# Optimization experiments

Hardware: AMD Instinct MI355X
Metric: run time of the kernel (lower is better)

## Reference

```python
import jax, jax.numpy as jnp
import numpy as np

B, T, H, I, O = 2048, 256, 256, 64, 64  # batch, seq_len, hidden, input(=output) dim


def setup_inputs() -> dict:
    key = jax.random.key(0)
    ks = jax.random.split(key, 14)
    def w(k, shape, fan):
        return jax.random.normal(k, shape, jnp.float32) / np.float32(np.sqrt(fan))
    return {
        "noise": jax.random.normal(ks[0], (B, I), jnp.float32),
        "W_ih0": w(ks[1], (3 * H, I), I),
        "W_hh0": w(ks[2], (3 * H, H), H),
        "b_ih0": w(ks[3], (3 * H,), H),
        "b_hh0": w(ks[4], (3 * H,), H),
        "W_ih12": w(ks[5], (2, 3 * H, H), H),
        "W_hh12": w(ks[6], (2, 3 * H, H), H),
        "b_ih12": w(ks[7], (2, 3 * H), H),
        "b_hh12": w(ks[8], (2, 3 * H), H),
        "W1": w(ks[9], (H, H), H),
        "b1": w(ks[10], (H,), H),
        "W2": w(ks[11], (O, H), H),
        "b2": w(ks[12], (O,), H),
        "seq_len": T,
    }


def _gru_cell(x, h, Wi, Wh, bi, bh):
    # PyTorch GRU cell, gate order (r, z, n)
    gi = x @ Wi.T + bi        # [B, 3H]
    gh = h @ Wh.T + bh        # [B, 3H]
    ir, iz, inn = jnp.split(gi, 3, axis=-1)
    hr, hz, hn = jnp.split(gh, 3, axis=-1)
    r = jax.nn.sigmoid(ir + hr)
    z = jax.nn.sigmoid(iz + hz)
    n = jnp.tanh(inn + r * hn)
    return (1.0 - z) * n + z * h


def reference(noise, W_ih0, W_hh0, b_ih0, b_hh0, W_ih12, W_hh12, b_ih12, b_hh12,
              W1, b1, W2, b2, seq_len):
    Bb = noise.shape[0]
    Hd = W_hh0.shape[1]
    h_init = jnp.zeros((3, Bb, Hd), noise.dtype)

    def step(carry, _):
        x, h = carry
        h0 = _gru_cell(x, h[0], W_ih0, W_hh0, b_ih0, b_hh0)
        h1 = _gru_cell(h0, h[1], W_ih12[0], W_hh12[0], b_ih12[0], b_hh12[0])
        h2 = _gru_cell(h1, h[2], W_ih12[1], W_hh12[1], b_ih12[1], b_hh12[1])
        # output MLP: Linear -> ReLU -> Linear -> Tanh; fed back as next input
        y = jnp.tanh(jax.nn.relu(h2 @ W1.T + b1) @ W2.T + b2)  # [B, O]
        return (y, jnp.stack([h0, h1, h2])), y

    _, ys = jax.lax.scan(step, (noise, h_init), None, length=seq_len)
    return jnp.transpose(ys, (1, 0, 2))  # [B, T, O]
```

## Files before the change

kernel.cpp:

```cpp
#include <hip/hip_runtime.h>
#include <hip/hip_bf16.h>


typedef __attribute__((ext_vector_type(8))) short short8;
typedef __attribute__((ext_vector_type(4))) float f32x4;

#define TT   256
#define NTHR 512
#define NBLK 256

#define FB_WI0  0
#define FB_WH0  6144
#define FB_WI1  30720
#define FB_WH1  55296
#define FB_WI2  79872
#define FB_WH2  104448
#define FB_W1   129024
#define FB_W2   137216
#define TOTAL_FRAGS 139264

#define OFF_FLAGS 2228224u
#define OFF_H0    (OFF_FLAGS + 4096u)
#define OFF_H1    (OFF_H0 + 1048576u)
#define OFF_H2    (OFF_H1 + 1048576u)
#define OFF_A1    (OFF_H2 + 1048576u)
#define OFF_Y     (OFF_A1 + 1048576u)

#define WH0_F 0
#define WI1_F 24
#define WH1_F 48
#define WI2_F 72
#define WH2_F 96
#define W2_F  120
#define XW_F  152

__device__ __forceinline__ short bf16_rne(float v) {
  union { float f; unsigned u; } c; c.f = v;
  unsigned u = c.u;
  u += 0x7FFFu + ((u >> 16) & 1u);
  return (short)(u >> 16);
}
__device__ __forceinline__ float fast_sigmoid(float x) {
  return 1.0f / (1.0f + __expf(-x));
}
__device__ __forceinline__ float fast_tanh(float x) {
  return 1.0f - 2.0f / (__expf(2.0f * x) + 1.0f);
}

__device__ __forceinline__ void gll(const short* src, short* ldst) {
  __builtin_amdgcn_global_load_lds(
      (const __attribute__((address_space(1))) void*)src,
      (__attribute__((address_space(3))) void*)ldst, 16, 0, 0);
}
__device__ __forceinline__ void vm0() {
  asm volatile("s_waitcnt vmcnt(0)" ::: "memory");
  __builtin_amdgcn_sched_barrier(0);
}

__device__ __forceinline__ void gstore_ic(short* g, short v) {
  asm volatile("global_store_short %0, %1, off sc0 sc1" :: "v"(g), "v"(v) : "memory");
}

__device__ __forceinline__ void gather8_ic(const short* base, short8 (&f)[8]) {
  asm volatile(
      "global_load_dwordx4 %0, %8, off sc0 sc1\n\t"
      "global_load_dwordx4 %1, %8, off offset:64 sc0 sc1\n\t"
      "global_load_dwordx4 %2, %8, off offset:128 sc0 sc1\n\t"
      "global_load_dwordx4 %3, %8, off offset:192 sc0 sc1\n\t"
      "global_load_dwordx4 %4, %8, off offset:256 sc0 sc1\n\t"
      "global_load_dwordx4 %5, %8, off offset:320 sc0 sc1\n\t"
      "global_load_dwordx4 %6, %8, off offset:384 sc0 sc1\n\t"
      "global_load_dwordx4 %7, %8, off offset:448 sc0 sc1\n\t"
      "s_waitcnt vmcnt(0)"
      : "=&v"(f[0]), "=&v"(f[1]), "=&v"(f[2]), "=&v"(f[3]),
        "=&v"(f[4]), "=&v"(f[5]), "=&v"(f[6]), "=&v"(f[7])
      : "v"(base) : "memory");
}

__device__ __forceinline__ void gather2_l2(const short* base, short8& a, short8& b) {
  asm volatile(
      "global_load_dwordx4 %0, %2, off sc0\n\t"
      "global_load_dwordx4 %1, %2, off offset:64 sc0\n\t"
      "s_waitcnt vmcnt(0)"
      : "=&v"(a), "=&v"(b) : "v"(base) : "memory");
}

__device__ __forceinline__ void flag_add(unsigned* f) {
  unsigned one = 1u;
  asm volatile("global_atomic_add %0, %1, off sc1" :: "v"(f), "v"(one) : "memory");
}
__device__ __forceinline__ unsigned flag_read(unsigned* f) {
  unsigned v;
  asm volatile("global_load_dword %0, %1, off sc0 sc1\n\ts_waitcnt vmcnt(0)"
               : "=&v"(v) : "v"(f) : "memory");
  return v;
}

__device__ __forceinline__ void group_sync(unsigned* flag, unsigned target) {
  vm0();
  __syncthreads();
  if (threadIdx.x == 0) {
    flag_add(flag);
    while (flag_read(flag) < target) __builtin_amdgcn_s_sleep(1);
  }
  __syncthreads();
}

struct CB4 { float brz, bzz, bin, bhn; };
__device__ __forceinline__ CB4 make_cb4(const float* bi, const float* bh, int col) {
  CB4 cb;
  cb.brz = bi[col] + bh[col];
  cb.bzz = bi[256 + col] + bh[256 + col];
  cb.bin = bi[512 + col];
  cb.bhn = bh[512 + col];
  return cb;
}

__global__ void pack_weights(const float* __restrict__ Wi0, const float* __restrict__ Wh0,
                             const float* __restrict__ Wih12, const float* __restrict__ Whh12,
                             const float* __restrict__ W1, const float* __restrict__ W2,
                             short* __restrict__ outp)
{
  int f = blockIdx.x * blockDim.x + threadIdx.x;
  if (f >= TOTAL_FRAGS) return;
  const float* src; int K; int rel;
  if (f < FB_WH0)        { src = Wi0;            K = 64;  rel = f; }
  else if (f < FB_WI1)   { src = Wh0;            K = 256; rel = f - FB_WH0; }
  else if (f < FB_WH1)   { src = Wih12;          K = 256; rel = f - FB_WI1; }
  else if (f < FB_WI2)   { src = Whh12;          K = 256; rel = f - FB_WH1; }
  else if (f < FB_WH2)   { src = Wih12 + 196608; K = 256; rel = f - FB_WI2; }
  else if (f < FB_W1)    { src = Whh12 + 196608; K = 256; rel = f - FB_WH2; }
  else if (f < FB_W2)    { src = W1;             K = 256; rel = f - FB_W1; }
  else                   { src = W2;             K = 256; rel = f - FB_W2; }
  int lane = rel & 63;
  int q = rel >> 6;
  int KT = K >> 5;
  int kt = q % KT;
  int nt = q / KT;
  int n  = nt * 16 + (lane & 15);
  int k0 = kt * 32 + (lane >> 4) * 8;
  short8 v;
#pragma unroll
  for (int e = 0; e < 8; ++e) v[e] = bf16_rne(src[(size_t)n * K + k0 + e]);
  *(short8*)(outp + (size_t)f * 8) = v;
}

__global__ void zero_flags(unsigned* f) {
  if (threadIdx.x < 1024) f[threadIdx.x] = 0u;
}

#define MFMA(a, b, acc) __builtin_amdgcn_mfma_f32_16x16x32_bf16((a), (b), (acc), 0, 0, 0)
#define LDSF(idx) (*(const short8*)(wlds + (idx) * 512 + lane * 8))

#define GATE_UPDATE(agi, agh, cb, hm, hg)                                    \
  _Pragma("unroll") for (int j = 0; j < 4; ++j) {                            \
    float r_ = fast_sigmoid(agi[0][j] + agh[0][j] + cb.brz);                 \
    float z_ = fast_sigmoid(agi[1][j] + agh[1][j] + cb.bzz);                 \
    float n_ = fast_tanh(agi[2][j] + cb.bin + r_ * (agh[2][j] + cb.bhn));    \
    float h_ = n_ + z_ * (hm[j] - n_);                                       \
    hm[j] = h_;                                                              \
    gstore_ic(hg + (size_t)(grow0 + lhi * 4 + j) * 256 + col, bf16_rne(h_)); \
  }

__global__ __launch_bounds__(NTHR, 2)
void timegan_shard(const float* __restrict__ noise, char* __restrict__ ws,
                   const float* __restrict__ b_ih0, const float* __restrict__ b_hh0,
                   const float* __restrict__ b_ih12, const float* __restrict__ b_hh12,
                   const float* __restrict__ b1v, const float* __restrict__ b2v,
                   float* __restrict__ out)
{
  __shared__ __align__(16) short wlds[158 * 512];

  const short* wpack = (const short*)ws;
  unsigned* flags = (unsigned*)(ws + OFF_FLAGS);
  short* h0g = (short*)(ws + OFF_H0);
  short* h1g = (short*)(ws + OFF_H1);
  short* h2g = (short*)(ws + OFF_H2);
  short* a1g = (short*)(ws + OFF_A1);
  short* yg  = (short*)(ws + OFF_Y);

  const int tid = threadIdx.x;
  const int lane = tid & 63, w = tid >> 6;
  const int l15 = lane & 15, lhi = lane >> 4;
  const int gg = blockIdx.x & 15;
  const int m  = blockIdx.x >> 4;
  const int grow0 = gg * 128 + w * 16;
  const int col = m * 16 + l15;
  unsigned* gflag = flags + gg * 8;
  short* ybb = yg + (size_t)blockIdx.x * 128 * 64;

  if (w == 0) {
    int dst = 0;
    const int fbs[5] = {FB_WH0, FB_WI1, FB_WH1, FB_WI2, FB_WH2};
    for (int s = 0; s < 5; ++s)
      for (int g = 0; g < 3; ++g)
        for (int kt = 0; kt < 8; ++kt) {
          gll(wpack + ((size_t)fbs[s] + (size_t)((g * 16 + m) * 8 + kt) * 64 + lane) * 8,
              wlds + dst * 512);
          ++dst;
        }
    for (int nt = 0; nt < 4; ++nt)
      for (int kt = 0; kt < 8; ++kt) {
        gll(wpack + ((size_t)FB_W2 + (nt * 8 + kt) * 64 + lane) * 8, wlds + dst * 512);
        ++dst;
      }
    for (int g = 0; g < 3; ++g)
      for (int kt = 0; kt < 2; ++kt) {
        gll(wpack + ((size_t)FB_WI0 + ((g * 16 + m) * 2 + kt) * 64 + lane) * 8,
            wlds + dst * 512);
        ++dst;
      }
  }

  short8 w1f[8];
#pragma unroll
  for (int kt = 0; kt < 8; ++kt)
    w1f[kt] = *(const short8*)(wpack + ((size_t)FB_W1 + (m * 8 + kt) * 64 + lane) * 8);

  short8 xf[2];
  {
    const float* np = noise + (size_t)(grow0 + l15) * 64;
#pragma unroll
    for (int kt = 0; kt < 2; ++kt) {
      f32x4 u0 = *(const f32x4*)(np + kt * 32 + lhi * 8);
      f32x4 u1 = *(const f32x4*)(np + kt * 32 + lhi * 8 + 4);
      short8 v;
#pragma unroll
      for (int e = 0; e < 4; ++e) { v[e] = bf16_rne(u0[e]); v[4 + e] = bf16_rne(u1[e]); }
      xf[kt] = v;
    }
  }

  CB4 cb0 = make_cb4(b_ih0, b_hh0, col);
  CB4 cb1 = make_cb4(b_ih12, b_hh12, col);
  CB4 cb2 = make_cb4(b_ih12 + 768, b_hh12 + 768, col);
  float bm1 = b1v[col];
  float bm2v[4];
#pragma unroll
  for (int nt = 0; nt < 4; ++nt) bm2v[nt] = b2v[nt * 16 + l15];

  short8 h0f[8], h1f[8], h2f[8];
  float hm0[4], hm1[4], hm2[4];
  {
    short8 z8 = {0, 0, 0, 0, 0, 0, 0, 0};
#pragma unroll
    for (int kt = 0; kt < 8; ++kt) { h0f[kt] = z8; h1f[kt] = z8; h2f[kt] = z8; }
#pragma unroll
    for (int j = 0; j < 4; ++j) { hm0[j] = 0.f; hm1[j] = 0.f; hm2[j] = 0.f; }
  }

  vm0();
  __syncthreads();

  const f32x4 z4 = {0.f, 0.f, 0.f, 0.f};
  const int rowoff = (grow0 + l15) * 256 + lhi * 8;

#pragma unroll 1
  for (int t = 0; t < TT; ++t) {
    const unsigned tgt = 16u * (unsigned)(t + 1);

    {
      f32x4 agi[3] = {z4, z4, z4}, agh[3] = {z4, z4, z4};
#pragma unroll
      for (int g = 0; g < 3; ++g) {
        agi[g] = MFMA(xf[0], LDSF(XW_F + g * 2 + 0), agi[g]);
        agi[g] = MFMA(xf[1], LDSF(XW_F + g * 2 + 1), agi[g]);
      }
#pragma unroll
      for (int kt = 0; kt < 8; ++kt)
#pragma unroll
        for (int g = 0; g < 3; ++g)
          agh[g] = MFMA(h0f[kt], LDSF(WH0_F + g * 8 + kt), agh[g]);
      GATE_UPDATE(agi, agh, cb0, hm0, h0g)
    }
    group_sync(gflag + 0, tgt);
    gather8_ic(h0g + rowoff, h0f);

    {
      f32x4 agi[3] = {z4, z4, z4}, agh[3] = {z4, z4, z4};
#pragma unroll
      for (int kt = 0; kt < 8; ++kt)
#pragma unroll
        for (int g = 0; g < 3; ++g) {
          agi[g] = MFMA(h0f[kt], LDSF(WI1_F + g * 8 + kt), agi[g]);
          agh[g] = MFMA(h1f[kt], LDSF(WH1_F + g * 8 + kt), agh[g]);
        }
      GATE_UPDATE(agi, agh, cb1, hm1, h1g)
    }
    group_sync(gflag + 1, tgt);
    gather8_ic(h1g + rowoff, h1f);

    {
      f32x4 agi[3] = {z4, z4, z4}, agh[3] = {z4, z4, z4};
#pragma unroll
      for (int kt = 0; kt < 8; ++kt)
#pragma unroll
        for (int g = 0; g < 3; ++g) {
          agi[g] = MFMA(h1f[kt], LDSF(WI2_F + g * 8 + kt), agi[g]);
          agh[g] = MFMA(h2f[kt], LDSF(WH2_F + g * 8 + kt), agh[g]);
        }
      GATE_UPDATE(agi, agh, cb2, hm2, h2g)
    }
    group_sync(gflag + 2, tgt);
    gather8_ic(h2g + rowoff, h2f);

    {
      f32x4 am = z4;
#pragma unroll
      for (int kt = 0; kt < 8; ++kt) am = MFMA(h2f[kt], w1f[kt], am);
#pragma unroll
      for (int j = 0; j < 4; ++j) {
        float v = fmaxf(am[j] + bm1, 0.f);
        gstore_ic(a1g + (size_t)(grow0 + lhi * 4 + j) * 256 + col, bf16_rne(v));
      }
    }
    group_sync(gflag + 3, tgt);
    short8 af[8];
    gather8_ic(a1g + rowoff, af);

#pragma unroll
    for (int nt = 0; nt < 4; ++nt) {
      f32x4 ay = z4;
#pragma unroll
      for (int kt = 0; kt < 8; ++kt) ay = MFMA(af[kt], LDSF(W2_F + nt * 8 + kt), ay);
#pragma unroll
      for (int j = 0; j < 4; ++j) {
        int grow = grow0 + lhi * 4 + j;
        float y = fast_tanh(ay[j] + bm2v[nt]);
        if (m == 0) out[((size_t)grow * TT + t) * 64 + nt * 16 + l15] = y;
        ybb[(w * 16 + lhi * 4 + j) * 64 + nt * 16 + l15] = bf16_rne(y);
      }
    }
    if (t < TT - 1) {
      vm0();
      gather2_l2(ybb + (w * 16 + l15) * 64 + lhi * 8, xf[0], xf[1]);
    }
  }
}

extern "C" void kernel_launch(void* const* d_in, const int* in_sizes, int n_in,
                              void* d_out, int out_size, void* d_ws, size_t ws_size,
                              hipStream_t stream)
{
  const float* noise  = (const float*)d_in[0];
  const float* W_ih0  = (const float*)d_in[1];
  const float* W_hh0  = (const float*)d_in[2];
  const float* b_ih0  = (const float*)d_in[3];
  const float* b_hh0  = (const float*)d_in[4];
  const float* W_ih12 = (const float*)d_in[5];
  const float* W_hh12 = (const float*)d_in[6];
  const float* b_ih12 = (const float*)d_in[7];
  const float* b_hh12 = (const float*)d_in[8];
  const float* W1     = (const float*)d_in[9];
  const float* b1     = (const float*)d_in[10];
  const float* W2     = (const float*)d_in[11];
  const float* b2     = (const float*)d_in[12];
  float* out = (float*)d_out;
  char* ws = (char*)d_ws;
  short* wpack = (short*)d_ws;

  zero_flags<<<1, 1024, 0, stream>>>((unsigned*)(ws + OFF_FLAGS));
  pack_weights<<<(TOTAL_FRAGS + 255) / 256, 256, 0, stream>>>(
      W_ih0, W_hh0, W_ih12, W_hh12, W1, W2, wpack);

  timegan_shard<<<NBLK, NTHR, 0, stream>>>(
      noise, ws, b_ih0, b_hh0, b_ih12, b_hh12, b1, b2, out);
}
```

Measured before the change: 5.470 ms.

## Use XCC-local L2 atomics for group barriers when the group shares one XCC

At startup each block records its hardware XCC id. Each 16-block group then checks whether all its members run on the same XCC. If they do, the per-step barriers use device-scope L2 atomics (add plus an atomic read-back of zero) measured against a captured base value, instead of system-coherent atomics and bypassing loads. Flag counters are also spread to separate cache lines. This aims to cut the latency of the four inter-block barriers per timestep, at the cost of an extra init handshake and two template instantiations of the main loop.

After: 5.208 ms. 4.8% less time.

```diff
diff --git a/kernel.cpp b/kernel.cpp
--- a/kernel.cpp
+++ b/kernel.cpp
@@ -20,7 +20,7 @@
 #define TOTAL_FRAGS 139264
 
 #define OFF_FLAGS 2228224u
-#define OFF_H0    (OFF_FLAGS + 4096u)
+#define OFF_H0    (OFF_FLAGS + 16384u)
 #define OFF_H1    (OFF_H0 + 1048576u)
 #define OFF_H2    (OFF_H1 + 1048576u)
 #define OFF_A1    (OFF_H2 + 1048576u)
@@ -60,7 +60,6 @@
 __device__ __forceinline__ void gstore_ic(short* g, short v) {
   asm volatile("global_store_short %0, %1, off sc0 sc1" :: "v"(g), "v"(v) : "memory");
 }
-
 __device__ __forceinline__ void gather8_ic(const short* base, short8 (&f)[8]) {
   asm volatile(
       "global_load_dwordx4 %0, %8, off sc0 sc1\n\t"
@@ -76,7 +75,6 @@
         "=&v"(f[4]), "=&v"(f[5]), "=&v"(f[6]), "=&v"(f[7])
       : "v"(base) : "memory");
 }
-
 __device__ __forceinline__ void gather2_l2(const short* base, short8& a, short8& b) {
   asm volatile(
       "global_load_dwordx4 %0, %2, off sc0\n\t"
@@ -84,24 +82,43 @@
       "s_waitcnt vmcnt(0)"
       : "=&v"(a), "=&v"(b) : "v"(base) : "memory");
 }
-
-__device__ __forceinline__ void flag_add(unsigned* f) {
+__device__ __forceinline__ void flag_add_ic(unsigned* f) {
   unsigned one = 1u;
   asm volatile("global_atomic_add %0, %1, off sc1" :: "v"(f), "v"(one) : "memory");
 }
-__device__ __forceinline__ unsigned flag_read(unsigned* f) {
+__device__ __forceinline__ unsigned flag_read_ic(unsigned* f) {
   unsigned v;
   asm volatile("global_load_dword %0, %1, off sc0 sc1\n\ts_waitcnt vmcnt(0)"
                : "=&v"(v) : "v"(f) : "memory");
   return v;
 }
-
-__device__ __forceinline__ void group_sync(unsigned* flag, unsigned target) {
+__device__ __forceinline__ void group_sync_ic(unsigned* flag, unsigned target) {
   vm0();
   __syncthreads();
   if (threadIdx.x == 0) {
-    flag_add(flag);
-    while (flag_read(flag) < target) __builtin_amdgcn_s_sleep(1);
+    flag_add_ic(flag);
+    while (flag_read_ic(flag) < target) __builtin_amdgcn_s_sleep(1);
+  }
+  __syncthreads();
+}
+
+__device__ __forceinline__ void flag_add_l2(unsigned* f) {
+  unsigned one = 1u;
+  asm volatile("global_atomic_add %0, %1, off" :: "v"(f), "v"(one) : "memory");
+}
+__device__ __forceinline__ unsigned flag_rmwread_l2(unsigned* f) {
+  unsigned v; unsigned zero = 0u;
+  asm volatile("global_atomic_add %0, %1, %2, off sc0\n\ts_waitcnt vmcnt(0)"
+               : "=&v"(v) : "v"(f), "v"(zero) : "memory");
+  return v;
+}
+__device__ __forceinline__ void group_sync_fast(unsigned* flag, unsigned base,
+                                                unsigned delta) {
+  vm0();
+  __syncthreads();
+  if (threadIdx.x == 0) {
+    flag_add_l2(flag);
+    while (flag_rmwread_l2(flag) - base < delta) __builtin_amdgcn_s_sleep(1);
   }
   __syncthreads();
 }
@@ -146,7 +163,9 @@
 }
 
 __global__ void zero_flags(unsigned* f) {
-  if (threadIdx.x < 1024) f[threadIdx.x] = 0u;
+  int i = threadIdx.x;
+#pragma unroll
+  for (int k = 0; k < 4; ++k) f[i + 1024 * k] = 0u;
 }
 
 #define MFMA(a, b, acc) __builtin_amdgcn_mfma_f32_16x16x32_bf16((a), (b), (acc), 0, 0, 0)
@@ -162,6 +181,108 @@
     gstore_ic(hg + (size_t)(grow0 + lhi * 4 + j) * 256 + col, bf16_rne(h_)); \
   }
 
+#define BARRIER(p)                                                            \
+  do {                                                                        \
+    if constexpr (FAST) group_sync_fast(fsl + (p), bs[p], 16u * (t + 1));     \
+    else                group_sync_ic(isl + (p), 16u * (t + 1));              \
+  } while (0)
+
+template<bool FAST>
+__device__ void mainloop(
+    const short* wlds,
+    short* h0g, short* h1g, short* h2g, short* a1g, short* ybb,
+    float* __restrict__ out,
+    unsigned* fsl, unsigned* isl, const unsigned* bs,
+    short8 (&xf)[2], short8 (&h0f)[8], short8 (&h1f)[8], short8 (&h2f)[8],
+    short8 (&w1f)[8],
+    float (&hm0)[4], float (&hm1)[4], float (&hm2)[4],
+    const CB4 cb0, const CB4 cb1, const CB4 cb2,
+    float bm1, const float (&bm2v)[4],
+    int grow0, int col, int rowoff, int lane, int l15, int lhi, int w, int m)
+{
+  const f32x4 z4 = {0.f, 0.f, 0.f, 0.f};
+
+#pragma unroll 1
+  for (unsigned t = 0; t < TT; ++t) {
+    {
+      f32x4 agi[3] = {z4, z4, z4}, agh[3] = {z4, z4, z4};
+#pragma unroll
+      for (int g = 0; g < 3; ++g) {
+        agi[g] = MFMA(xf[0], LDSF(XW_F + g * 2 + 0), agi[g]);
+        agi[g] = MFMA(xf[1], LDSF(XW_F + g * 2 + 1), agi[g]);
+      }
+#pragma unroll
+      for (int kt = 0; kt < 8; ++kt)
+#pragma unroll
+        for (int g = 0; g < 3; ++g)
+          agh[g] = MFMA(h0f[kt], LDSF(WH0_F + g * 8 + kt), agh[g]);
+      GATE_UPDATE(agi, agh, cb0, hm0, h0g)
+    }
+    BARRIER(0);
+    gather8_ic(h0g + rowoff, h0f);
+
+    {
+      f32x4 agi[3] = {z4, z4, z4}, agh[3] = {z4, z4, z4};
+#pragma unroll
+      for (int kt = 0; kt < 8; ++kt)
+#pragma unroll
+        for (int g = 0; g < 3; ++g) {
+          agi[g] = MFMA(h0f[kt], LDSF(WI1_F + g * 8 + kt), agi[g]);
+          agh[g] = MFMA(h1f[kt], LDSF(WH1_F + g * 8 + kt), agh[g]);
+        }
+      GATE_UPDATE(agi, agh, cb1, hm1, h1g)
+    }
+    BARRIER(1);
+    gather8_ic(h1g + rowoff, h1f);
+
+    {
+      f32x4 agi[3] = {z4, z4, z4}, agh[3] = {z4, z4, z4};
+#pragma unroll
+      for (int kt = 0; kt < 8; ++kt)
+#pragma unroll
+        for (int g = 0; g < 3; ++g) {
+          agi[g] = MFMA(h1f[kt], LDSF(WI2_F + g * 8 + kt), agi[g]);
+          agh[g] = MFMA(h2f[kt], LDSF(WH2_F + g * 8 + kt), agh[g]);
+        }
+      GATE_UPDATE(agi, agh, cb2, hm2, h2g)
+    }
+    BARRIER(2);
+    gather8_ic(h2g + rowoff, h2f);
+
+    {
+      f32x4 am = z4;
+#pragma unroll
+      for (int kt = 0; kt < 8; ++kt) am = MFMA(h2f[kt], w1f[kt], am);
+#pragma unroll
+      for (int j = 0; j < 4; ++j) {
+        float v = fmaxf(am[j] + bm1, 0.f);
+        gstore_ic(a1g + (size_t)(grow0 + lhi * 4 + j) * 256 + col, bf16_rne(v));
+      }
+    }
+    BARRIER(3);
+    short8 af[8];
+    gather8_ic(a1g + rowoff, af);
+
+#pragma unroll
+    for (int nt = 0; nt < 4; ++nt) {
+      f32x4 ay = z4;
+#pragma unroll
+      for (int kt = 0; kt < 8; ++kt) ay = MFMA(af[kt], LDSF(W2_F + nt * 8 + kt), ay);
+#pragma unroll
+      for (int j = 0; j < 4; ++j) {
+        int grow = grow0 + lhi * 4 + j;
+        float y = fast_tanh(ay[j] + bm2v[nt]);
+        if (m == 0) out[((size_t)grow * TT + t) * 64 + nt * 16 + l15] = y;
+        ybb[(w * 16 + lhi * 4 + j) * 64 + nt * 16 + l15] = bf16_rne(y);
+      }
+    }
+    if (t < TT - 1) {
+      vm0();
+      gather2_l2(ybb + (w * 16 + l15) * 64 + lhi * 8, xf[0], xf[1]);
+    }
+  }
+}
+
 __global__ __launch_bounds__(NTHR, 2)
 void timegan_shard(const float* __restrict__ noise, char* __restrict__ ws,
                    const float* __restrict__ b_ih0, const float* __restrict__ b_hh0,
@@ -170,6 +291,8 @@
                    float* __restrict__ out)
 {
   __shared__ __align__(16) short wlds[158 * 512];
+  __shared__ int fastsh;
+  __shared__ unsigned bsh[4];
 
   const short* wpack = (const short*)ws;
   unsigned* flags = (unsigned*)(ws + OFF_FLAGS);
@@ -182,12 +305,17 @@
   const int tid = threadIdx.x;
   const int lane = tid & 63, w = tid >> 6;
   const int l15 = lane & 15, lhi = lane >> 4;
-  const int gg = blockIdx.x & 15;
-  const int m  = blockIdx.x >> 4;
+  const int bid = blockIdx.x;
+  const int gg = bid & 15;
+  const int m  = bid >> 4;
   const int grow0 = gg * 128 + w * 16;
   const int col = m * 16 + l15;
-  unsigned* gflag = flags + gg * 8;
-  short* ybb = yg + (size_t)blockIdx.x * 128 * 64;
+  unsigned* fsl    = flags + gg * 64;
+  unsigned* isl    = flags + 1024 + gg * 8;
+  unsigned* initA  = flags + 1280 + gg * 16;
+  unsigned* initB  = initA + 1;
+  unsigned* xccids = flags + 1792;
+  short* ybb = yg + (size_t)bid * 128 * 64;
 
   if (w == 0) {
     int dst = 0;
@@ -249,93 +377,45 @@
     for (int j = 0; j < 4; ++j) { hm0[j] = 0.f; hm1[j] = 0.f; hm2[j] = 0.f; }
   }
 
-  vm0();
+  if (tid == 0) {
+    unsigned xcc = 0;
+    asm volatile("s_getreg_b32 %0, hwreg(HW_REG_XCC_ID)" : "=s"(xcc));
+    unsigned* myid = xccids + bid;
+    unsigned xv = xcc;
+    asm volatile("global_store_dword %0, %1, off sc0 sc1" :: "v"(myid), "v"(xv) : "memory");
+  }
+  group_sync_ic(initA, 16u);
+
+  if (tid < 64) {
+    unsigned* xp = xccids + gg + 16 * (lane & 15);
+    unsigned xv;
+    asm volatile("global_load_dword %0, %1, off sc0 sc1\n\ts_waitcnt vmcnt(0)"
+                 : "=&v"(xv) : "v"(xp) : "memory");
+    unsigned ref = __shfl(xv, 0);
+    int ok = __all(xv == ref);
+    if (lane == 0) fastsh = ok;
+  }
   __syncthreads();
 
-  const f32x4 z4 = {0.f, 0.f, 0.f, 0.f};
+  if (tid == 0 && fastsh) {
+#pragma unroll
+    for (int p = 0; p < 4; ++p) bsh[p] = flag_rmwread_l2(fsl + p);
+  }
+  group_sync_ic(initB, 16u);
+
+  const bool fast = fastsh != 0;
   const int rowoff = (grow0 + l15) * 256 + lhi * 8;
 
-#pragma unroll 1
-  for (int t = 0; t < TT; ++t) {
-    const unsigned tgt = 16u * (unsigned)(t + 1);
-
-    {
-      f32x4 agi[3] = {z4, z4, z4}, agh[3] = {z4, z4, z4};
-#pragma unroll
-      for (int g = 0; g < 3; ++g) {
-        agi[g] = MFMA(xf[0], LDSF(XW_F + g * 2 + 0), agi[g]);
-        agi[g] = MFMA(xf[1], LDSF(XW_F + g * 2 + 1), agi[g]);
-      }
-#pragma unroll
-      for (int kt = 0; kt < 8; ++kt)
-#pragma unroll
-        for (int g = 0; g < 3; ++g)
-          agh[g] = MFMA(h0f[kt], LDSF(WH0_F + g * 8 + kt), agh[g]);
-      GATE_UPDATE(agi, agh, cb0, hm0, h0g)
-    }
-    group_sync(gflag + 0, tgt);
-    gather8_ic(h0g + rowoff, h0f);
-
-    {
-      f32x4 agi[3] = {z4, z4, z4}, agh[3] = {z4, z4, z4};
-#pragma unroll
-      for (int kt = 0; kt < 8; ++kt)
-#pragma unroll
-        for (int g = 0; g < 3; ++g) {
-          agi[g] = MFMA(h0f[kt], LDSF(WI1_F + g * 8 + kt), agi[g]);
-          agh[g] = MFMA(h1f[kt], LDSF(WH1_F + g * 8 + kt), agh[g]);
-        }
-      GATE_UPDATE(agi, agh, cb1, hm1, h1g)
-    }
-    group_sync(gflag + 1, tgt);
-    gather8_ic(h1g + rowoff, h1f);
-
-    {
-      f32x4 agi[3] = {z4, z4, z4}, agh[3] = {z4, z4, z4};
-#pragma unroll
-      for (int kt = 0; kt < 8; ++kt)
-#pragma unroll
-        for (int g = 0; g < 3; ++g) {
-          agi[g] = MFMA(h1f[kt], LDSF(WI2_F + g * 8 + kt), agi[g]);
-          agh[g] = MFMA(h2f[kt], LDSF(WH2_F + g * 8 + kt), agh[g]);
-        }
-      GATE_UPDATE(agi, agh, cb2, hm2, h2g)
-    }
-    group_sync(gflag + 2, tgt);
-    gather8_ic(h2g + rowoff, h2f);
-
-    {
-      f32x4 am = z4;
-#pragma unroll
-      for (int kt = 0; kt < 8; ++kt) am = MFMA(h2f[kt], w1f[kt], am);
-#pragma unroll
-      for (int j = 0; j < 4; ++j) {
-        float v = fmaxf(am[j] + bm1, 0.f);
-        gstore_ic(a1g + (size_t)(grow0 + lhi * 4 + j) * 256 + col, bf16_rne(v));
-      }
-    }
-    group_sync(gflag + 3, tgt);
-    short8 af[8];
-    gather8_ic(a1g + rowoff, af);
-
-#pragma unroll
-    for (int nt = 0; nt < 4; ++nt) {
-      f32x4 ay = z4;
-#pragma unroll
-      for (int kt = 0; kt < 8; ++kt) ay = MFMA(af[kt], LDSF(W2_F + nt * 8 + kt), ay);
-#pragma unroll
-      for (int j = 0; j < 4; ++j) {
-        int grow = grow0 + lhi * 4 + j;
-        float y = fast_tanh(ay[j] + bm2v[nt]);
-        if (m == 0) out[((size_t)grow * TT + t) * 64 + nt * 16 + l15] = y;
-        ybb[(w * 16 + lhi * 4 + j) * 64 + nt * 16 + l15] = bf16_rne(y);
-      }
-    }
-    if (t < TT - 1) {
-      vm0();
-      gather2_l2(ybb + (w * 16 + l15) * 64 + lhi * 8, xf[0], xf[1]);
-    }
-  }
+  if (fast)
+    mainloop<true>(wlds, h0g, h1g, h2g, a1g, ybb, out, fsl, isl, bsh,
+                   xf, h0f, h1f, h2f, w1f, hm0, hm1, hm2,
+                   cb0, cb1, cb2, bm1, bm2v,
+                   grow0, col, rowoff, lane, l15, lhi, w, m);
+  else
+    mainloop<false>(wlds, h0g, h1g, h2g, a1g, ybb, out, fsl, isl, bsh,
+                    xf, h0f, h1f, h2f, w1f, hm0, hm1, hm2,
+                    cb0, cb1, cb2, bm1, bm2v,
+                    grow0, col, rowoff, lane, l15, lhi, w, m);
 }
 
 extern "C" void kernel_launch(void* const* d_in, const int* in_sizes, int n_in,
```
